# Kernel optimization log

Hardware: AMD Instinct MI355X
Metric: run time of the kernel (lower is better)

Reference implementation:

```python
import jax, jax.numpy as jnp
import numpy as np


def setup_inputs() -> dict:
    key = jax.random.key(0)
    ks = jax.random.split(key, 7)
    B, T, C, H = 4, 4096, 1024, 64
    x = jax.random.normal(ks[0], (B, T, C), dtype=jnp.float32)
    Wq = jax.random.normal(ks[1], (C, H), dtype=jnp.float32) * 0.02
    bq = jax.random.normal(ks[2], (H,), dtype=jnp.float32) * 0.02
    Wk = jax.random.normal(ks[3], (C, H), dtype=jnp.float32) * 0.02
    bk = jax.random.normal(ks[4], (H,), dtype=jnp.float32) * 0.02
    Wv = jax.random.normal(ks[5], (C, H), dtype=jnp.float32) * 0.02
    bv = jax.random.normal(ks[6], (H,), dtype=jnp.float32) * 0.02
    return {"x": x, "Wq": Wq, "bq": bq, "Wk": Wk, "bk": bk, "Wv": Wv, "bv": bv}


def reference(x, Wq, bq, Wk, bk, Wv, bv):
    B, T, C = x.shape
    q = x @ Wq + bq            # [B,T,H]
    k = x @ Wk + bk            # [B,T,H]
    v = x @ Wv + bv            # [B,T,H]
    # NOTE: original scales by C**-0.5 where C = n_embd (input dim), not head_size
    scale = jnp.asarray(C, x.dtype) ** -0.5
    wei = jnp.einsum('bth,bsh->bts', q, k) * scale   # [B,T,T]
    causal = jnp.tril(jnp.ones((T, T), dtype=bool))
    wei = jnp.where(causal, wei, -jnp.inf)
    wei = jax.nn.softmax(wei, axis=-1)
    out = jnp.einsum('bts,bsh->bth', wei, v)         # [B,T,H]
    return out
```

## Files before the change

kernel.cpp:

```cpp
#include <hip/hip_runtime.h>
#include <hip/hip_bf16.h>

#define T_DIM 4096
#define C_DIM 1024
#define H_DIM 64
#define B_DIM 4

typedef __attribute__((ext_vector_type(8))) short short8v;
typedef __attribute__((ext_vector_type(4))) short short4v;
typedef __attribute__((ext_vector_type(4))) float float4v;

__device__ __forceinline__ unsigned short f2bf(float f) {
    __hip_bfloat16 h = __float2bfloat16(f);
    return *reinterpret_cast<unsigned short*>(&h);
}

__device__ __forceinline__ int vperm(int t5) {
    return ((t5 & 12) << 1) | (t5 & 3) | ((t5 & 16) >> 2);
}

#define GLL16(gsrc, ldst)                                                         \
    __builtin_amdgcn_global_load_lds(                                             \
        (const __attribute__((address_space(1))) unsigned int*)(gsrc),            \
        (__attribute__((address_space(3))) unsigned int*)(ldst), 16, 0, 0)

__global__ __launch_bounds__(256) void wprep(
    const float* __restrict__ Wq, const float* __restrict__ Wk,
    const float* __restrict__ Wv, unsigned short* __restrict__ wt)
{
    __shared__ float tile[64][65];
    const int t  = threadIdx.x;
    const int m  = blockIdx.x >> 4;
    const int k0 = (blockIdx.x & 15) * 64;
    const float* __restrict__ W = (m == 0) ? Wq : (m == 1) ? Wk : Wv;

    const int kr = t >> 4, c4 = (t & 15) * 4;
#pragma unroll
    for (int j = 0; j < 4; ++j) {
        const int row = kr + j * 16;
        const float4 v = *(const float4*)(W + (size_t)(k0 + row) * 64 + c4);
        tile[row][c4 + 0] = v.x; tile[row][c4 + 1] = v.y;
        tile[row][c4 + 2] = v.z; tile[row][c4 + 3] = v.w;
    }
    __syncthreads();

    const int col = t >> 2, q = t & 3;
    short8v s0, s1;
#pragma unroll
    for (int j = 0; j < 8; ++j) s0[j] = (short)f2bf(tile[q * 16 + j][col]);
#pragma unroll
    for (int j = 0; j < 8; ++j) s1[j] = (short)f2bf(tile[q * 16 + 8 + j][col]);
    unsigned short* dst = wt + (size_t)(m * 64 + col) * 1024 + k0 + q * 16;
    *(short8v*)dst = s0;
    *(short8v*)(dst + 8) = s1;
}

__global__ __launch_bounds__(512, 2) void qkv_gemm(
    const float* __restrict__ x, const unsigned short* __restrict__ wt,
    const float* __restrict__ bq, const float* __restrict__ bk,
    const float* __restrict__ bv,
    unsigned short* __restrict__ qb, unsigned short* __restrict__ kmat,
    unsigned short* __restrict__ vP)
{
    __shared__ __align__(16) unsigned char lx[2][4096];
    __shared__ __align__(16) unsigned char lw[2][24576];

    const int t    = threadIdx.x;
    const int lane = t & 63;
    const int w    = t >> 6;
    const int l15  = lane & 15;
    const int g4   = lane >> 4;
    const int r0   = blockIdx.x * 32;

    const int rg  = w & 1;
    const int cgr = (w >> 1) & 1;
    const int kh  = w >> 2;

    const int srow  = t >> 4;
    const int sq    = t & 15;
    const int xbyte = srow * 128 + ((sq >> 1) ^ (srow & 7)) * 16 + (sq & 1) * 8;
    const float* __restrict__ xsrc = x + (size_t)(r0 + srow) * C_DIM + sq * 4;
    const int wgs = (t & 7) ^ ((t >> 3) & 7);
    const unsigned char* __restrict__ wB = (const unsigned char*)wt;

    float4v acc[6];
#pragma unroll
    for (int cg = 0; cg < 6; ++cg) acc[cg] = (float4v){0.f, 0.f, 0.f, 0.f};

#define WSTAGE(p, kb)                                                             \
    {                                                                             \
        _Pragma("unroll")                                                         \
        for (int i = 0; i < 3; ++i)                                               \
            GLL16(wB + (size_t)(i * 64 + (t >> 3)) * 2048 + (kb) * 128 + wgs * 16,\
                  &lw[p][(i * 512 + t) * 16]);                                    \
    }
#define XCVT_WRITE(p, v)                                                          \
    {                                                                             \
        __hip_bfloat162 c0_ = __float22bfloat162_rn(make_float2((v).x, (v).y));   \
        __hip_bfloat162 c1_ = __float22bfloat162_rn(make_float2((v).z, (v).w));   \
        unsigned int* d_ = (unsigned int*)&lx[p][xbyte];                          \
        d_[0] = *(unsigned int*)&c0_;                                             \
        d_[1] = *(unsigned int*)&c1_;                                             \
    }

    float4 xvA, xvB;

    {
        const float4 x0 = *(const float4*)xsrc;
        WSTAGE(0, 0);
        __builtin_amdgcn_sched_barrier(0);
        xvA = *(const float4*)(xsrc + 64);
        XCVT_WRITE(0, x0);
        asm volatile("s_waitcnt vmcnt(1) lgkmcnt(0)" ::: "memory");
        __builtin_amdgcn_s_barrier();
        __builtin_amdgcn_sched_barrier(0);
    }

    const int arow = rg * 16 + l15;
    const int axor = arow & 7;
    const int kg   = kh * 4 + g4;

#pragma unroll
    for (int kb = 0; kb < 15; ++kb) {
        const int p = kb & 1;
        WSTAGE(p ^ 1, kb + 1);
        __builtin_amdgcn_sched_barrier(0);
        const int pf = (kb + 2 < 16) ? (kb + 2) : 15;
        if ((kb & 1) == 0) xvB = *(const float4*)(xsrc + pf * 64);
        else               xvA = *(const float4*)(xsrc + pf * 64);

        const short8v af = *(const short8v*)&lx[p][arow * 128 + (kg ^ axor) * 16];
#pragma unroll
        for (int cg = 0; cg < 6; ++cg) {
            const int col = cgr * 96 + cg * 16 + l15;
            const short8v bf =
                *(const short8v*)&lw[p][col * 128 + ((kg ^ (col & 7))) * 16];
            acc[cg] = __builtin_amdgcn_mfma_f32_16x16x32_bf16(af, bf, acc[cg], 0, 0, 0);
        }

        if ((kb & 1) == 0) { XCVT_WRITE(p ^ 1, xvA); }
        else               { XCVT_WRITE(p ^ 1, xvB); }

        asm volatile("s_waitcnt vmcnt(1) lgkmcnt(0)" ::: "memory");
        __builtin_amdgcn_s_barrier();
        __builtin_amdgcn_sched_barrier(0);
    }
    {
        const short8v af = *(const short8v*)&lx[1][arow * 128 + (kg ^ axor) * 16];
#pragma unroll
        for (int cg = 0; cg < 6; ++cg) {
            const int col = cgr * 96 + cg * 16 + l15;
            const short8v bf =
                *(const short8v*)&lw[1][col * 128 + ((kg ^ (col & 7))) * 16];
            acc[cg] = __builtin_amdgcn_mfma_f32_16x16x32_bf16(af, bf, acc[cg], 0, 0, 0);
        }
    }
    __syncthreads();

    float* comm = (float*)lw;
    if (kh == 1) {
        const int base = ((w - 4) * 64 + lane) * 24;
#pragma unroll
        for (int cg = 0; cg < 6; ++cg)
#pragma unroll
            for (int e = 0; e < 4; ++e) comm[base + cg * 4 + e] = acc[cg][e];
    }
    __syncthreads();
    if (kh == 0) {
        const int base = (w * 64 + lane) * 24;
#pragma unroll
        for (int cg = 0; cg < 6; ++cg)
#pragma unroll
            for (int e = 0; e < 4; ++e) acc[cg][e] += comm[base + cg * 4 + e];

        const float qs = 0.03125f * 1.44269504088896f;
#pragma unroll
        for (int cg = 0; cg < 6; ++cg) {
            const int cabs = cgr * 96 + cg * 16 + l15;
            const int m    = cabs >> 6;
            const int h    = cabs & 63;
            const float bb = ((m == 0) ? bq : (m == 1) ? bk : bv)[h];
#pragma unroll
            for (int rr = 0; rr < 4; ++rr) {
                const int row = r0 + rg * 16 + 4 * g4 + rr;
                const float vv = acc[cg][rr] + bb;
                if (m == 0) {
                    qb[(size_t)row * 64 + h] = f2bf(vv * qs);
                } else if (m == 1) {
                    kmat[(size_t)row * 64 + h] = f2bf(vv);
                } else {
                    const int b_i = row >> 12;
                    const int tt  = row & 4095;
                    const int tp  = (tt & ~31) | vperm(tt & 31);
                    vP[((size_t)b_i * 64 + h) * T_DIM + tp] = f2bf(vv);
                }
            }
        }
    }
#undef WSTAGE
#undef XCVT_WRITE
}

__global__ __launch_bounds__(512, 4) void attn_mfma(
    const unsigned short* __restrict__ qb, const unsigned short* __restrict__ kmat,
    const unsigned short* __restrict__ vP, float* __restrict__ out)
{
    __shared__ float partO[8][32][68];
    __shared__ float partl[8][32];

    const int w    = threadIdx.x >> 6;
    const int lane = threadIdx.x & 63;
    const int l15  = lane & 15;
    const int g    = lane >> 4;
    const int i    = blockIdx.x;
    const int p2   = (i & 255) >> 2;
    const int b    = i & 3;
    const int tt   = (i < 256) ? (127 - p2) : p2;
    const int q0   = tt * 32;
    const int n    = tt + 1;

    const unsigned short* __restrict__ qbase = qb + ((size_t)b * T_DIM + q0) * 64;
    short8v qf[2][2];
    qf[0][0] = *(const short8v*)(qbase + (size_t)l15 * 64 + 8 * g);
    qf[0][1] = *(const short8v*)(qbase + (size_t)l15 * 64 + 32 + 8 * g);
    qf[1][0] = *(const short8v*)(qbase + (size_t)(16 + l15) * 64 + 8 * g);
    qf[1][1] = *(const short8v*)(qbase + (size_t)(16 + l15) * 64 + 32 + 8 * g);

    const unsigned short* __restrict__ kbase = kmat + (size_t)b * T_DIM * 64;
    const unsigned short* __restrict__ vbase = vP + (size_t)b * 64 * T_DIM;

    short8v kones;
#pragma unroll
    for (int j = 0; j < 8; ++j) kones[j] = (short)0x3F80;

    float4v acc[2][4];
    float4v accl[2];
#pragma unroll
    for (int qt = 0; qt < 2; ++qt) {
#pragma unroll
        for (int f = 0; f < 4; ++f) acc[qt][f] = (float4v){0.f, 0.f, 0.f, 0.f};
        accl[qt] = (float4v){0.f, 0.f, 0.f, 0.f};
    }

    const int rem = n & 7;
    const int cnt = (n >> 3) + (w < rem ? 1 : 0);
    const int st  = w * (n >> 3) + (w < rem ? w : rem);

    for (int s = 0; s < cnt; ++s) {
        const int kv0 = (st + s) * 32;

        const unsigned short* kr0 = kbase + (size_t)(kv0 + l15) * 64 + 8 * g;
        const unsigned short* kr1 = kr0 + 16 * 64;
        const short8v ka0 = *(const short8v*)kr0;
        const short8v ka1 = *(const short8v*)(kr0 + 32);
        const short8v ka2 = *(const short8v*)kr1;
        const short8v ka3 = *(const short8v*)(kr1 + 32);

        short8v vb4[4];
#pragma unroll
        for (int f = 0; f < 4; ++f)
            vb4[f] = *(const short8v*)(
                vbase + (size_t)(f * 16 + l15) * T_DIM + kv0 + 8 * g);

#pragma unroll
        for (int qt = 0; qt < 2; ++qt) {
            const float4v z = (float4v){0.f, 0.f, 0.f, 0.f};
            float4v slo = __builtin_amdgcn_mfma_f32_16x16x32_bf16(ka0, qf[qt][0], z, 0, 0, 0);
            slo = __builtin_amdgcn_mfma_f32_16x16x32_bf16(ka1, qf[qt][1], slo, 0, 0, 0);
            float4v shi = __builtin_amdgcn_mfma_f32_16x16x32_bf16(ka2, qf[qt][0], z, 0, 0, 0);
            shi = __builtin_amdgcn_mfma_f32_16x16x32_bf16(ka3, qf[qt][1], shi, 0, 0, 0);

            float pl[4], ph[4];
            if (kv0 + 31 <= q0 + 16 * qt) {
#pragma unroll
                for (int r = 0; r < 4; ++r) {
                    pl[r] = exp2f(slo[r]);
                    ph[r] = exp2f(shi[r]);
                }
            } else {
                const int qabs = q0 + 16 * qt + l15;
#pragma unroll
                for (int r = 0; r < 4; ++r) {
                    const int kvlo = kv0 + 4 * g + r;
                    pl[r] = (kvlo <= qabs) ? exp2f(slo[r]) : 0.f;
                    ph[r] = (kvlo + 16 <= qabs) ? exp2f(shi[r]) : 0.f;
                }
            }
            short8v pa;
            {
                unsigned int* pu = (unsigned int*)&pa;
                __hip_bfloat162 c0 = __float22bfloat162_rn(make_float2(pl[0], pl[1]));
                __hip_bfloat162 c1 = __float22bfloat162_rn(make_float2(pl[2], pl[3]));
                __hip_bfloat162 c2 = __float22bfloat162_rn(make_float2(ph[0], ph[1]));
                __hip_bfloat162 c3 = __float22bfloat162_rn(make_float2(ph[2], ph[3]));
                pu[0] = *(unsigned int*)&c0;
                pu[1] = *(unsigned int*)&c1;
                pu[2] = *(unsigned int*)&c2;
                pu[3] = *(unsigned int*)&c3;
            }
#pragma unroll
            for (int f = 0; f < 4; ++f)
                acc[qt][f] = __builtin_amdgcn_mfma_f32_16x16x32_bf16(pa, vb4[f], acc[qt][f], 0, 0, 0);
            accl[qt] = __builtin_amdgcn_mfma_f32_16x16x32_bf16(pa, kones, accl[qt], 0, 0, 0);
        }
    }

#pragma unroll
    for (int qt = 0; qt < 2; ++qt)
#pragma unroll
        for (int f = 0; f < 4; ++f)
#pragma unroll
            for (int r = 0; r < 4; ++r)
                partO[w][16 * qt + 4 * g + r][16 * f + l15] = acc[qt][f][r];
    if (l15 == 0) {
#pragma unroll
        for (int qt = 0; qt < 2; ++qt)
#pragma unroll
            for (int r = 0; r < 4; ++r)
                partl[w][16 * qt + 4 * g + r] = accl[qt][r];
    }
    __syncthreads();

    const int row = threadIdx.x >> 4;
    const int c0  = (threadIdx.x & 15) * 4;
    float lt = 0.f;
#pragma unroll
    for (int ww = 0; ww < 8; ++ww) lt += partl[ww][row];
    const float inv = 1.f / lt;
    float4 o = make_float4(0.f, 0.f, 0.f, 0.f);
#pragma unroll
    for (int ww = 0; ww < 8; ++ww) {
        const float4 s = *(const float4*)&partO[ww][row][c0];
        o.x += s.x; o.y += s.y; o.z += s.z; o.w += s.w;
    }
    o.x *= inv; o.y *= inv; o.z *= inv; o.w *= inv;
    *(float4*)(out + ((size_t)b * T_DIM + q0 + row) * 64 + c0) = o;
}

extern "C" void kernel_launch(void* const* d_in, const int* in_sizes, int n_in,
                              void* d_out, int out_size, void* d_ws, size_t ws_size,
                              hipStream_t stream) {
    const float* x  = (const float*)d_in[0];
    const float* Wq = (const float*)d_in[1];
    const float* bq = (const float*)d_in[2];
    const float* Wk = (const float*)d_in[3];
    const float* bk = (const float*)d_in[4];
    const float* Wv = (const float*)d_in[5];
    const float* bv = (const float*)d_in[6];
    float* out = (float*)d_out;

    const size_t rows = (size_t)B_DIM * T_DIM;
    char* ws = (char*)d_ws;
    unsigned short* qb   = (unsigned short*)ws;
    unsigned short* kmat = qb + rows * H_DIM;
    unsigned short* vP   = kmat + rows * H_DIM;
    unsigned short* wt   = vP + rows * H_DIM;

    wprep<<<48, 256, 0, stream>>>(Wq, Wk, Wv, wt);
    qkv_gemm<<<512, 512, 0, stream>>>(x, wt, bq, bk, bv, qb, kmat, vP);
    attn_mfma<<<512, 512, 0, stream>>>(qb, kmat, vP, out);
}
```

Before: 62.00 us.

## Split attention into KV-chunked partials with LDS-staged K/V and combine kernel

Attention is restructured. Each block now handles 128 query rows over a KV chunk of at most 1024 keys. K and V tiles are staged into LDS through a 3-deep global_load_lds pipeline and shared by all 8 waves, where previously each wave reloaded K and V from global memory. Partial O and l results are written to workspace and summed by a new combine kernel. The QKV GEMM weight staging is also deepened from double to triple buffering. The aim is more K/V reuse and better balance across the causal triangle, at the cost of an extra launch and the partial-result traffic.

```diff
diff --git a/kernel.cpp b/kernel.cpp
--- a/kernel.cpp
+++ b/kernel.cpp
@@ -7,7 +7,6 @@
 #define B_DIM 4
 
 typedef __attribute__((ext_vector_type(8))) short short8v;
-typedef __attribute__((ext_vector_type(4))) short short4v;
 typedef __attribute__((ext_vector_type(4))) float float4v;
 
 __device__ __forceinline__ unsigned short f2bf(float f) {
@@ -17,6 +16,11 @@
 
 __device__ __forceinline__ int vperm(int t5) {
     return ((t5 & 12) << 1) | (t5 & 3) | ((t5 & 16) >> 2);
+}
+
+__device__ __forceinline__ int chunk_prefix(int t) {
+    const int g = t >> 3;
+    return t + 4 * g * (g - 1) + (t & 7) * g;
 }
 
 #define GLL16(gsrc, ldst)                                                         \
@@ -63,7 +67,7 @@
     unsigned short* __restrict__ vP)
 {
     __shared__ __align__(16) unsigned char lx[2][4096];
-    __shared__ __align__(16) unsigned char lw[2][24576];
+    __shared__ __align__(16) unsigned char lw[3][24576];
 
     const int t    = threadIdx.x;
     const int lane = t & 63;
@@ -108,10 +112,11 @@
     {
         const float4 x0 = *(const float4*)xsrc;
         WSTAGE(0, 0);
+        WSTAGE(1, 1);
         __builtin_amdgcn_sched_barrier(0);
         xvA = *(const float4*)(xsrc + 64);
         XCVT_WRITE(0, x0);
-        asm volatile("s_waitcnt vmcnt(1) lgkmcnt(0)" ::: "memory");
+        asm volatile("s_waitcnt vmcnt(4) lgkmcnt(0)" ::: "memory");
         __builtin_amdgcn_s_barrier();
         __builtin_amdgcn_sched_barrier(0);
     }
@@ -121,15 +126,15 @@
     const int kg   = kh * 4 + g4;
 
 #pragma unroll
-    for (int kb = 0; kb < 15; ++kb) {
-        const int p = kb & 1;
-        WSTAGE(p ^ 1, kb + 1);
+    for (int kb = 0; kb < 14; ++kb) {
+        const int p  = kb % 3;
+        const int ps = (kb + 2) % 3;
+        WSTAGE(ps, kb + 2);
         __builtin_amdgcn_sched_barrier(0);
-        const int pf = (kb + 2 < 16) ? (kb + 2) : 15;
-        if ((kb & 1) == 0) xvB = *(const float4*)(xsrc + pf * 64);
-        else               xvA = *(const float4*)(xsrc + pf * 64);
-
-        const short8v af = *(const short8v*)&lx[p][arow * 128 + (kg ^ axor) * 16];
+        if ((kb & 1) == 0) xvB = *(const float4*)(xsrc + (kb + 2) * 64);
+        else               xvA = *(const float4*)(xsrc + (kb + 2) * 64);
+
+        const short8v af = *(const short8v*)&lx[kb & 1][arow * 128 + (kg ^ axor) * 16];
 #pragma unroll
         for (int cg = 0; cg < 6; ++cg) {
             const int col = cgr * 96 + cg * 16 + l15;
@@ -138,20 +143,34 @@
             acc[cg] = __builtin_amdgcn_mfma_f32_16x16x32_bf16(af, bf, acc[cg], 0, 0, 0);
         }
 
-        if ((kb & 1) == 0) { XCVT_WRITE(p ^ 1, xvA); }
-        else               { XCVT_WRITE(p ^ 1, xvB); }
-
-        asm volatile("s_waitcnt vmcnt(1) lgkmcnt(0)" ::: "memory");
+        if ((kb & 1) == 0) { XCVT_WRITE((kb + 1) & 1, xvA); }
+        else               { XCVT_WRITE((kb + 1) & 1, xvB); }
+
+        asm volatile("s_waitcnt vmcnt(4) lgkmcnt(0)" ::: "memory");
         __builtin_amdgcn_s_barrier();
         __builtin_amdgcn_sched_barrier(0);
     }
     {
-        const short8v af = *(const short8v*)&lx[1][arow * 128 + (kg ^ axor) * 16];
+        const short8v af = *(const short8v*)&lx[0][arow * 128 + (kg ^ axor) * 16];
 #pragma unroll
         for (int cg = 0; cg < 6; ++cg) {
             const int col = cgr * 96 + cg * 16 + l15;
             const short8v bf =
-                *(const short8v*)&lw[1][col * 128 + ((kg ^ (col & 7))) * 16];
+                *(const short8v*)&lw[2][col * 128 + ((kg ^ (col & 7))) * 16];
+            acc[cg] = __builtin_amdgcn_mfma_f32_16x16x32_bf16(af, bf, acc[cg], 0, 0, 0);
+        }
+        XCVT_WRITE(1, xvA);
+        asm volatile("s_waitcnt vmcnt(0) lgkmcnt(0)" ::: "memory");
+        __builtin_amdgcn_s_barrier();
+        __builtin_amdgcn_sched_barrier(0);
+    }
+    {
+        const short8v af = *(const short8v*)&lx[1][arow * 128 + (kg ^ axor) * 16];
+#pragma unroll
+        for (int cg = 0; cg < 6; ++cg) {
+            const int col = cgr * 96 + cg * 16 + l15;
+            const short8v bf =
+                *(const short8v*)&lw[0][col * 128 + ((kg ^ (col & 7))) * 16];
             acc[cg] = __builtin_amdgcn_mfma_f32_16x16x32_bf16(af, bf, acc[cg], 0, 0, 0);
         }
     }
@@ -201,98 +220,118 @@
 #undef XCVT_WRITE
 }
 
-__global__ __launch_bounds__(512, 4) void attn_mfma(
+__global__ __launch_bounds__(512, 4) void attn_part(
     const unsigned short* __restrict__ qb, const unsigned short* __restrict__ kmat,
-    const unsigned short* __restrict__ vP, float* __restrict__ out)
+    const unsigned short* __restrict__ vP, float* __restrict__ pO,
+    float* __restrict__ pl)
 {
-    __shared__ float partO[8][32][68];
-    __shared__ float partl[8][32];
-
-    const int w    = threadIdx.x >> 6;
-    const int lane = threadIdx.x & 63;
+    __shared__ __align__(16) unsigned char lk[3][4096];
+    __shared__ __align__(16) unsigned char lv[3][4096];
+
+    const int tid  = threadIdx.x;
+    const int w    = tid >> 6;
+    const int lane = tid & 63;
     const int l15  = lane & 15;
     const int g    = lane >> 4;
-    const int i    = blockIdx.x;
-    const int p2   = (i & 255) >> 2;
-    const int b    = i & 3;
-    const int tt   = (i < 256) ? (127 - p2) : p2;
-    const int q0   = tt * 32;
-    const int n    = tt + 1;
-
-    const unsigned short* __restrict__ qbase = qb + ((size_t)b * T_DIM + q0) * 64;
-    short8v qf[2][2];
-    qf[0][0] = *(const short8v*)(qbase + (size_t)l15 * 64 + 8 * g);
-    qf[0][1] = *(const short8v*)(qbase + (size_t)l15 * 64 + 32 + 8 * g);
-    qf[1][0] = *(const short8v*)(qbase + (size_t)(16 + l15) * 64 + 8 * g);
-    qf[1][1] = *(const short8v*)(qbase + (size_t)(16 + l15) * 64 + 32 + 8 * g);
-
-    const unsigned short* __restrict__ kbase = kmat + (size_t)b * T_DIM * 64;
-    const unsigned short* __restrict__ vbase = vP + (size_t)b * 64 * T_DIM;
+
+    const int b   = blockIdx.x & 3;
+    const int idx = 79 - (blockIdx.x >> 2);
+    int t = 0;
+    for (int tt = 1; tt < 32; ++tt)
+        if (chunk_prefix(tt) <= idx) t = tt;
+    const int c    = idx - chunk_prefix(t);
+    const int q0   = t * 128;
+    const int kv_l = q0 + 128;
+    const int d0   = c * 1024;
+    const int dend = (d0 + 1024 < kv_l) ? (d0 + 1024) : kv_l;
+    const int ns   = (dend - d0) >> 5;
+    const int slot = b * 80 + idx;
+
+    const unsigned char* kB = (const unsigned char*)kmat + (size_t)b * T_DIM * 128;
+    const unsigned char* vB = (const unsigned char*)vP + (size_t)b * 64 * T_DIM * 2;
+    const bool isK = tid < 256;
+    const int krow = tid >> 3, kdg = tid & 7;
+    const int u = tid & 255, vh = u >> 2, vdg = u & 3;
+    const unsigned char* ksrc = kB + krow * 128 + ((kdg ^ (krow & 7)) * 16);
+    const unsigned char* vsrc = vB + (size_t)vh * 8192 + ((vdg ^ (vh & 3)) * 16);
+    const int kdst = tid * 16;
+    const int vdst = u * 16;
+
+#define STAGE(p, ss)                                                          \
+    {                                                                         \
+        const int off_ = d0 + (ss) * 32;                                      \
+        if (isK) GLL16(ksrc + (size_t)off_ * 128, &lk[p][kdst]);              \
+        else     GLL16(vsrc + (size_t)off_ * 2,   &lv[p][vdst]);              \
+    }
+
+    const unsigned short* qrow = qb + ((size_t)b * T_DIM + q0 + 16 * w + l15) * 64;
+    const short8v qf0 = *(const short8v*)(qrow + 8 * g);
+    const short8v qf1 = *(const short8v*)(qrow + 32 + 8 * g);
 
     short8v kones;
 #pragma unroll
     for (int j = 0; j < 8; ++j) kones[j] = (short)0x3F80;
 
-    float4v acc[2][4];
-    float4v accl[2];
-#pragma unroll
-    for (int qt = 0; qt < 2; ++qt) {
-#pragma unroll
-        for (int f = 0; f < 4; ++f) acc[qt][f] = (float4v){0.f, 0.f, 0.f, 0.f};
-        accl[qt] = (float4v){0.f, 0.f, 0.f, 0.f};
-    }
-
-    const int rem = n & 7;
-    const int cnt = (n >> 3) + (w < rem ? 1 : 0);
-    const int st  = w * (n >> 3) + (w < rem ? w : rem);
-
-    for (int s = 0; s < cnt; ++s) {
-        const int kv0 = (st + s) * 32;
-
-        const unsigned short* kr0 = kbase + (size_t)(kv0 + l15) * 64 + 8 * g;
-        const unsigned short* kr1 = kr0 + 16 * 64;
-        const short8v ka0 = *(const short8v*)kr0;
-        const short8v ka1 = *(const short8v*)(kr0 + 32);
-        const short8v ka2 = *(const short8v*)kr1;
-        const short8v ka3 = *(const short8v*)(kr1 + 32);
-
-        short8v vb4[4];
-#pragma unroll
-        for (int f = 0; f < 4; ++f)
-            vb4[f] = *(const short8v*)(
-                vbase + (size_t)(f * 16 + l15) * T_DIM + kv0 + 8 * g);
-
-#pragma unroll
-        for (int qt = 0; qt < 2; ++qt) {
+    float4v acc[4];
+    float4v accl = (float4v){0.f, 0.f, 0.f, 0.f};
+#pragma unroll
+    for (int f = 0; f < 4; ++f) acc[f] = (float4v){0.f, 0.f, 0.f, 0.f};
+
+    const int qmax = q0 + 16 * w + 15;
+    const int kxor = l15 & 7;
+    const int vxor = l15 & 3;
+
+    STAGE(0, 0);
+    STAGE(1, (ns > 1) ? 1 : 0);
+    asm volatile("s_waitcnt vmcnt(1)" ::: "memory");
+    __builtin_amdgcn_s_barrier();
+
+    int p = 0;
+    for (int s = 0; s < ns; ++s) {
+        const int ps = (p + 2 >= 3) ? (p - 1) : (p + 2);
+        const int sn = (s + 2 < ns) ? (s + 2) : (ns - 1);
+        STAGE(ps, sn);
+
+        const int kv0 = d0 + s * 32;
+        if (kv0 <= qmax) {
+            const short8v ka0 = *(const short8v*)&lk[p][(l15 * 8 + (g ^ kxor)) * 16];
+            const short8v ka1 = *(const short8v*)&lk[p][(l15 * 8 + ((4 + g) ^ kxor)) * 16];
+            const short8v ka2 = *(const short8v*)&lk[p][((16 + l15) * 8 + (g ^ kxor)) * 16];
+            const short8v ka3 = *(const short8v*)&lk[p][((16 + l15) * 8 + ((4 + g) ^ kxor)) * 16];
+            short8v vb[4];
+#pragma unroll
+            for (int f = 0; f < 4; ++f)
+                vb[f] = *(const short8v*)&lv[p][((f * 16 + l15) * 4 + (g ^ vxor)) * 16];
+
             const float4v z = (float4v){0.f, 0.f, 0.f, 0.f};
-            float4v slo = __builtin_amdgcn_mfma_f32_16x16x32_bf16(ka0, qf[qt][0], z, 0, 0, 0);
-            slo = __builtin_amdgcn_mfma_f32_16x16x32_bf16(ka1, qf[qt][1], slo, 0, 0, 0);
-            float4v shi = __builtin_amdgcn_mfma_f32_16x16x32_bf16(ka2, qf[qt][0], z, 0, 0, 0);
-            shi = __builtin_amdgcn_mfma_f32_16x16x32_bf16(ka3, qf[qt][1], shi, 0, 0, 0);
-
-            float pl[4], ph[4];
-            if (kv0 + 31 <= q0 + 16 * qt) {
+            float4v slo = __builtin_amdgcn_mfma_f32_16x16x32_bf16(ka0, qf0, z, 0, 0, 0);
+            slo = __builtin_amdgcn_mfma_f32_16x16x32_bf16(ka1, qf1, slo, 0, 0, 0);
+            float4v shi = __builtin_amdgcn_mfma_f32_16x16x32_bf16(ka2, qf0, z, 0, 0, 0);
+            shi = __builtin_amdgcn_mfma_f32_16x16x32_bf16(ka3, qf1, shi, 0, 0, 0);
+
+            float pl_[4], ph_[4];
+            if (kv0 + 31 <= q0 + 16 * w) {
 #pragma unroll
                 for (int r = 0; r < 4; ++r) {
-                    pl[r] = exp2f(slo[r]);
-                    ph[r] = exp2f(shi[r]);
+                    pl_[r] = exp2f(slo[r]);
+                    ph_[r] = exp2f(shi[r]);
                 }
             } else {
-                const int qabs = q0 + 16 * qt + l15;
+                const int qabs = q0 + 16 * w + l15;
 #pragma unroll
                 for (int r = 0; r < 4; ++r) {
                     const int kvlo = kv0 + 4 * g + r;
-                    pl[r] = (kvlo <= qabs) ? exp2f(slo[r]) : 0.f;
-                    ph[r] = (kvlo + 16 <= qabs) ? exp2f(shi[r]) : 0.f;
+                    pl_[r] = (kvlo <= qabs) ? exp2f(slo[r]) : 0.f;
+                    ph_[r] = (kvlo + 16 <= qabs) ? exp2f(shi[r]) : 0.f;
                 }
             }
             short8v pa;
             {
                 unsigned int* pu = (unsigned int*)&pa;
-                __hip_bfloat162 c0 = __float22bfloat162_rn(make_float2(pl[0], pl[1]));
-                __hip_bfloat162 c1 = __float22bfloat162_rn(make_float2(pl[2], pl[3]));
-                __hip_bfloat162 c2 = __float22bfloat162_rn(make_float2(ph[0], ph[1]));
-                __hip_bfloat162 c3 = __float22bfloat162_rn(make_float2(ph[2], ph[3]));
+                __hip_bfloat162 c0 = __float22bfloat162_rn(make_float2(pl_[0], pl_[1]));
+                __hip_bfloat162 c1 = __float22bfloat162_rn(make_float2(pl_[2], pl_[3]));
+                __hip_bfloat162 c2 = __float22bfloat162_rn(make_float2(ph_[0], ph_[1]));
+                __hip_bfloat162 c3 = __float22bfloat162_rn(make_float2(ph_[2], ph_[3]));
                 pu[0] = *(unsigned int*)&c0;
                 pu[1] = *(unsigned int*)&c1;
                 pu[2] = *(unsigned int*)&c2;
@@ -300,41 +339,55 @@
             }
 #pragma unroll
             for (int f = 0; f < 4; ++f)
-                acc[qt][f] = __builtin_amdgcn_mfma_f32_16x16x32_bf16(pa, vb4[f], acc[qt][f], 0, 0, 0);
-            accl[qt] = __builtin_amdgcn_mfma_f32_16x16x32_bf16(pa, kones, accl[qt], 0, 0, 0);
+                acc[f] = __builtin_amdgcn_mfma_f32_16x16x32_bf16(pa, vb[f], acc[f], 0, 0, 0);
+            accl = __builtin_amdgcn_mfma_f32_16x16x32_bf16(pa, kones, accl, 0, 0, 0);
         }
-    }
-
-#pragma unroll
-    for (int qt = 0; qt < 2; ++qt)
-#pragma unroll
-        for (int f = 0; f < 4; ++f)
-#pragma unroll
-            for (int r = 0; r < 4; ++r)
-                partO[w][16 * qt + 4 * g + r][16 * f + l15] = acc[qt][f][r];
+
+        asm volatile("s_waitcnt vmcnt(1) lgkmcnt(0)" ::: "memory");
+        __builtin_amdgcn_s_barrier();
+        p = (p + 1 >= 3) ? 0 : (p + 1);
+    }
+
+    float* po = pO + (size_t)slot * 8192 + (size_t)(16 * w) * 64;
+#pragma unroll
+    for (int f = 0; f < 4; ++f)
+#pragma unroll
+        for (int r = 0; r < 4; ++r)
+            po[(4 * g + r) * 64 + f * 16 + l15] = acc[f][r];
     if (l15 == 0) {
 #pragma unroll
-        for (int qt = 0; qt < 2; ++qt)
-#pragma unroll
-            for (int r = 0; r < 4; ++r)
-                partl[w][16 * qt + 4 * g + r] = accl[qt][r];
-    }
-    __syncthreads();
-
-    const int row = threadIdx.x >> 4;
-    const int c0  = (threadIdx.x & 15) * 4;
-    float lt = 0.f;
-#pragma unroll
-    for (int ww = 0; ww < 8; ++ww) lt += partl[ww][row];
-    const float inv = 1.f / lt;
+        for (int r = 0; r < 4; ++r)
+            pl[(size_t)slot * 128 + 16 * w + 4 * g + r] = accl[r];
+    }
+#undef STAGE
+}
+
+__global__ __launch_bounds__(256) void attn_comb(
+    const float* __restrict__ pO, const float* __restrict__ pl,
+    float* __restrict__ out)
+{
+    const int tid  = blockIdx.x * 256 + threadIdx.x;
+    const int row  = tid >> 4;
+    const int h4   = (tid & 15) * 4;
+    const int b    = row >> 12;
+    const int brow = row & 4095;
+    const int t    = brow >> 7;
+    const int rr   = brow & 127;
+    const int nc   = 1 + (t >> 3);
+    const int base = b * 80 + chunk_prefix(t);
+
+    const float* src  = pO + (size_t)base * 8192 + rr * 64 + h4;
+    const float* lsrc = pl + (size_t)base * 128 + rr;
     float4 o = make_float4(0.f, 0.f, 0.f, 0.f);
-#pragma unroll
-    for (int ww = 0; ww < 8; ++ww) {
-        const float4 s = *(const float4*)&partO[ww][row][c0];
+    float l = 0.f;
+    for (int c = 0; c < nc; ++c) {
+        const float4 s = *(const float4*)(src + (size_t)c * 8192);
         o.x += s.x; o.y += s.y; o.z += s.z; o.w += s.w;
-    }
+        l += lsrc[(size_t)c * 128];
+    }
+    const float inv = 1.f / l;
     o.x *= inv; o.y *= inv; o.z *= inv; o.w *= inv;
-    *(float4*)(out + ((size_t)b * T_DIM + q0 + row) * 64 + c0) = o;
+    *(float4*)(out + (size_t)row * 64 + h4) = o;
 }
 
 extern "C" void kernel_launch(void* const* d_in, const int* in_sizes, int n_in,
@@ -349,14 +402,16 @@
     const float* bv = (const float*)d_in[6];
     float* out = (float*)d_out;
 
-    const size_t rows = (size_t)B_DIM * T_DIM;
     char* ws = (char*)d_ws;
-    unsigned short* qb   = (unsigned short*)ws;
-    unsigned short* kmat = qb + rows * H_DIM;
-    unsigned short* vP   = kmat + rows * H_DIM;
-    unsigned short* wt   = vP + rows * H_DIM;
+    unsigned short* qb   = (unsigned short*)(ws);
+    unsigned short* kmat = (unsigned short*)(ws + (2u << 20));
+    unsigned short* vP   = (unsigned short*)(ws + (4u << 20));
+    unsigned short* wt   = (unsigned short*)(ws + (6u << 20));
+    float*          pO   = (float*)(ws + (8u << 20));
+    float*          pl   = (float*)(ws + (8u << 20) + 10485760u);
 
     wprep<<<48, 256, 0, stream>>>(Wq, Wk, Wv, wt);
     qkv_gemm<<<512, 512, 0, stream>>>(x, wt, bq, bk, bv, qb, kmat, vP);
-    attn_mfma<<<512, 512, 0, stream>>>(qb, kmat, vP, out);
-}
+    attn_part<<<320, 512, 0, stream>>>(qb, kmat, vP, pO, pl);
+    attn_comb<<<1024, 256, 0, stream>>>(pO, pl, out);
+}
```

Result: no change. 63.00 us (+1.6%).
